# Optimization experiments

Measured on AMD Instinct MI355X. Metric: run time of the kernel, lower is better.

The kernel has to match this reference:

```python
import jax, jax.numpy as jnp
import numpy as np

B, S, D, H = 2, 2048, 768, 12
DK = D // H
NEG = -1000000000.0


def setup_inputs() -> dict:
    key = jax.random.key(0)
    ks = jax.random.split(key, 12)
    inp = {
        "query": jax.random.normal(ks[0], (B, S, D), jnp.float32),
        "key": jax.random.normal(ks[1], (B, S, D), jnp.float32),
        "value": jax.random.normal(ks[2], (B, S, D), jnp.float32),
        "mask": jax.random.randint(ks[3], (B, 1, 1, S), 0, 2, jnp.int32),
    }
    sc = 1.0 / np.sqrt(D)
    inp["Wq"] = jax.random.normal(ks[4], (D, D), jnp.float32) * sc
    inp["bq"] = jnp.zeros((D,), jnp.float32)
    inp["Wk"] = jax.random.normal(ks[5], (D, D), jnp.float32) * sc
    inp["bk"] = jnp.zeros((D,), jnp.float32)
    inp["Wv"] = jax.random.normal(ks[6], (D, D), jnp.float32) * sc
    inp["bv"] = jnp.zeros((D,), jnp.float32)
    inp["Wo"] = jax.random.normal(ks[7], (D, D), jnp.float32) * sc
    inp["bo"] = jnp.zeros((D,), jnp.float32)
    return inp


def reference(query, key, value, mask, Wq, bq, Wk, bk, Wv, bv, Wo, bo):
    b = query.shape[0]
    # QKV projections -> [B, H, S, DK]
    def proj(x, W, bias):
        y = jnp.einsum('bsd,de->bse', x, W.T) + bias
        return y.reshape(b, -1, H, DK).transpose(0, 2, 1, 3)
    q = proj(query, Wq, bq)
    k = proj(key, Wk, bk)
    v = proj(value, Wv, bv)
    # scores: [B, H, S, S]
    scores = jnp.einsum('bhqd,bhkd->bhqk', q, k) / jnp.sqrt(jnp.float32(DK))
    scores = jnp.where(mask == 0, jnp.float32(NEG), scores)
    p = jax.nn.softmax(scores, axis=-1)
    x = jnp.einsum('bhqk,bhkd->bhqd', p, v)  # [B, H, S, DK]
    x = x.transpose(0, 2, 1, 3).reshape(b, -1, H * DK)
    return jnp.einsum('bsd,de->bse', x, Wo.T) + bo
```

## Files before the change

kernel.cpp:

```cpp
#include <hip/hip_runtime.h>

typedef unsigned short u16;
typedef __attribute__((ext_vector_type(8))) __bf16 bf16x8;
typedef __attribute__((ext_vector_type(8))) short s16x8;
typedef __attribute__((ext_vector_type(8))) unsigned short u16x8;
typedef __attribute__((ext_vector_type(4))) float f32x4;
typedef __attribute__((ext_vector_type(4))) unsigned short u16x4;
typedef __attribute__((ext_vector_type(4))) float fl4;

#define MFMA(a, b, c) __builtin_amdgcn_mfma_f32_16x16x32_bf16((a), (b), (c), 0, 0, 0)
#define QSC 0.18033688011112042f

__device__ __forceinline__ u16 f2bf(float f) {
  union { float f; unsigned u; } v; v.f = f;
  unsigned u = v.u;
  return (u16)((u + 0x7fffu + ((u >> 16) & 1u)) >> 16);
}

__device__ __forceinline__ float bf2f(u16 u) {
  union { unsigned u; float f; } v; v.u = ((unsigned)u) << 16;
  return v.f;
}

__device__ __forceinline__ void gll16(const u16* g, u16* l) {
  typedef __attribute__((address_space(1))) unsigned int gu32;
  typedef __attribute__((address_space(3))) unsigned int lu32;
  __builtin_amdgcn_global_load_lds((gu32*)g, (lu32*)l, 16, 0, 0);
}


__global__ __launch_bounds__(256) void k_convert_x(
    const float* __restrict__ q, const float* __restrict__ k,
    const float* __restrict__ v, u16* __restrict__ xb) {
  const int NG = 4096 * 768 / 4;
  const int n = 3 * NG;
  for (int i = blockIdx.x * 256 + threadIdx.x; i < n; i += gridDim.x * 256) {
    int seg = i / NG;
    int j = (i - seg * NG) * 4;
    const float* s = (seg == 0) ? q : ((seg == 1) ? k : v);
    fl4 f = *(const fl4*)(s + j);
    u16x4 o;
    o[0] = f2bf(f[0]); o[1] = f2bf(f[1]); o[2] = f2bf(f[2]); o[3] = f2bf(f[3]);
    *(u16x4*)(xb + seg * (4096 * 768) + j) = o;
  }
}

__global__ __launch_bounds__(256) void k_convert_w(
    const float* __restrict__ Wq, const float* __restrict__ Wk,
    const float* __restrict__ Wv, const float* __restrict__ Wo,
    u16* __restrict__ wqkv, u16* __restrict__ wob) {
  const int n = 3072 * 192;
  for (int i = blockIdx.x * 256 + threadIdx.x; i < n; i += gridDim.x * 256) {
    int row = i / 192;
    int col = (i - row * 192) * 4;
    const float* src; u16* dst; float sc = 1.0f;
    if (row < 768)       { src = Wq + row * 768;          dst = wqkv + row * 768; sc = QSC; }
    else if (row < 1536) { src = Wk + (row - 768) * 768;  dst = wqkv + row * 768; }
    else if (row < 2304) { src = Wv + (row - 1536) * 768; dst = wqkv + row * 768; }
    else                 { src = Wo + (row - 2304) * 768; dst = wob + (row - 2304) * 768; }
    fl4 f = *(const fl4*)(src + col);
    u16x4 o;
    o[0] = f2bf(f[0] * sc); o[1] = f2bf(f[1] * sc);
    o[2] = f2bf(f[2] * sc); o[3] = f2bf(f[3] * sc);
    *(u16x4*)(dst + col) = o;
  }
}


__global__ __launch_bounds__(256) void k_gemm_qkv(
    const u16* __restrict__ xb, const u16* __restrict__ wqkv,
    const float* __restrict__ bq, const float* __restrict__ bk_,
    const float* __restrict__ bv_,
    u16* __restrict__ Qb, u16* __restrict__ Kb, u16* __restrict__ Vtb) {
  __shared__ __align__(16) u16 As[128 * 32];
  __shared__ __align__(16) u16 Bs[128 * 32];
  const int tid = threadIdx.x;
  const int row0 = blockIdx.x * 128, col0 = blockIdx.y * 128;
  const int seg = col0 / 768;
  const u16* A = xb + (size_t)seg * (4096 * 768);
  const int w = tid >> 6, lane = tid & 63, lr = lane & 15, kg = lane >> 4;
  const int wr = (w >> 1) * 64, wc = (w & 1) * 64;

  const int c0 = tid, c1 = tid + 256;
  const int r0c = c0 >> 2, p0 = c0 & 3, g0 = p0 ^ ((r0c >> 1) & 3);
  const int r1c = c1 >> 2, p1 = c1 & 3, g1 = p1 ^ ((r1c >> 1) & 3);

  f32x4 acc[4][4];
  f32x4 zero = {0.f, 0.f, 0.f, 0.f};
#pragma unroll
  for (int i = 0; i < 4; i++)
#pragma unroll
    for (int j = 0; j < 4; j++) acc[i][j] = zero;

  int aoff[4], boff[4];
#pragma unroll
  for (int mi = 0; mi < 4; mi++) {
    int r = wr + mi * 16 + lr;
    aoff[mi] = r * 32 + (kg ^ ((r >> 1) & 3)) * 8;
  }
#pragma unroll
  for (int ni = 0; ni < 4; ni++) {
    int r = wc + ni * 16 + lr;
    boff[ni] = r * 32 + (kg ^ ((r >> 1) & 3)) * 8;
  }

  for (int kt = 0; kt < 24; kt++) {
    const int k0 = kt * 32;
    gll16(A + (row0 + r0c) * 768 + k0 + g0 * 8, As + c0 * 8);
    gll16(A + (row0 + r1c) * 768 + k0 + g1 * 8, As + c1 * 8);
    gll16(wqkv + (col0 + r0c) * 768 + k0 + g0 * 8, Bs + c0 * 8);
    gll16(wqkv + (col0 + r1c) * 768 + k0 + g1 * 8, Bs + c1 * 8);
    __syncthreads();
    bf16x8 af[4], bfr[4];
#pragma unroll
    for (int mi = 0; mi < 4; mi++) af[mi] = *(const bf16x8*)(As + aoff[mi]);
#pragma unroll
    for (int ni = 0; ni < 4; ni++) bfr[ni] = *(const bf16x8*)(Bs + boff[ni]);
#pragma unroll
    for (int mi = 0; mi < 4; mi++)
#pragma unroll
      for (int ni = 0; ni < 4; ni++)
        acc[mi][ni] = MFMA(af[mi], bfr[ni], acc[mi][ni]);
    __syncthreads();
  }

  const float* bias = (seg == 0) ? bq : ((seg == 1) ? bk_ : bv_);
  const float bsc = (seg == 0) ? QSC : 1.0f;
  const int ncol0 = col0 - seg * 768;
#pragma unroll
  for (int ni = 0; ni < 4; ni++) {
    const int n = ncol0 + wc + ni * 16 + lr;
    const float bval = bias[n] * bsc;
    const int hh = n >> 6, dk = n & 63;
#pragma unroll
    for (int mi = 0; mi < 4; mi++)
#pragma unroll
      for (int j = 0; j < 4; j++) {
        const int m = row0 + wr + mi * 16 + kg * 4 + j;
        const int bb = m >> 11, ss = m & 2047;
        const u16 val = f2bf(acc[mi][ni][j] + bval);
        if (seg == 0)
          Qb[((size_t)((bb * 12 + hh) * 2048 + ss)) * 64 + dk] = val;
        else if (seg == 1)
          Kb[((size_t)((bb * 12 + hh) * 2048 + ss)) * 64 + dk] = val;
        else
          Vtb[((size_t)((bb * 12 + hh) * 64 + dk)) * 2048 + ss] = val;
      }
  }
}


__global__ __launch_bounds__(256) void k_attn(
    const u16* __restrict__ Qb, const u16* __restrict__ Kb,
    const u16* __restrict__ Vtb, const int* __restrict__ mask,
    u16* __restrict__ o_part, float* __restrict__ l_part) {
  __shared__ __align__(16) u16 Ks[64 * 64];
  __shared__ __align__(16) u16 Vs[64 * 64];
  __shared__ __align__(16) u16 Ps[4][32 * 64];
  const int bh = blockIdx.y, b = bh / 12;
  const int half = blockIdx.z;
  const int kvb = half << 10;
  const int tid = threadIdx.x, w = tid >> 6, lane = tid & 63;
  const int lr = lane & 15, g = lane >> 4;
  const int q0 = blockIdx.x * 128 + w * 32;
  const u16* Qh = Qb + (size_t)bh * (2048 * 64);
  const u16* Kh = Kb + (size_t)bh * (2048 * 64);
  const u16* Vh = Vtb + (size_t)bh * (64 * 2048);
  const int* mb = mask + b * 2048;
  u16* Pw = Ps[w];

  bf16x8 aq[2][2];
#pragma unroll
  for (int mi = 0; mi < 2; mi++)
#pragma unroll
    for (int ks = 0; ks < 2; ks++)
      aq[mi][ks] = *(const bf16x8*)(Qh + (q0 + mi * 16 + lr) * 64 + ks * 32 + g * 8);

  f32x4 zero = {0.f, 0.f, 0.f, 0.f};
  f32x4 o[2][4];
#pragma unroll
  for (int mi = 0; mi < 2; mi++)
#pragma unroll
    for (int di = 0; di < 4; di++) o[mi][di] = zero;
  f32x4 o_l[2];
  o_l[0] = zero; o_l[1] = zero;

  s16x8 ov = {0x3F80, 0x3F80, 0x3F80, 0x3F80, 0x3F80, 0x3F80, 0x3F80, 0x3F80};
  bf16x8 ones = __builtin_bit_cast(bf16x8, ov);

  const int c0 = tid, c1 = tid + 256;
  const int sr0 = c0 >> 3, sg0 = (c0 & 7) ^ (sr0 & 7);
  const int sr1 = c1 >> 3, sg1 = (c1 & 7) ^ (sr1 & 7);

  for (int t = 0; t < 16; t++) {
    const int kv0 = kvb + t * 64;
    gll16(Kh + (kv0 + sr0) * 64 + sg0 * 8, Ks + c0 * 8);
    gll16(Kh + (kv0 + sr1) * 64 + sg1 * 8, Ks + c1 * 8);
    gll16(Vh + sr0 * 2048 + kv0 + sg0 * 8, Vs + c0 * 8);
    gll16(Vh + sr1 * 2048 + kv0 + sg1 * 8, Vs + c1 * 8);
    __syncthreads();

    f32x4 s[2][4];
#pragma unroll
    for (int ni = 0; ni < 4; ni++) {
      const int row = ni * 16 + lr;
      bf16x8 b0 = *(const bf16x8*)(Ks + row * 64 + ((g ^ (row & 7)) << 3));
      bf16x8 b1 = *(const bf16x8*)(Ks + row * 64 + (((4 + g) ^ (row & 7)) << 3));
#pragma unroll
      for (int mi = 0; mi < 2; mi++) {
        f32x4 z = zero;
        z = MFMA(aq[mi][0], b0, z);
        z = MFMA(aq[mi][1], b1, z);
        s[mi][ni] = z;
      }
    }
    int mk[4];
#pragma unroll
    for (int ni = 0; ni < 4; ni++) mk[ni] = mb[kv0 + ni * 16 + lr];
#pragma unroll
    for (int mi = 0; mi < 2; mi++)
#pragma unroll
      for (int ni = 0; ni < 4; ni++)
#pragma unroll
        for (int j = 0; j < 4; j++)
          s[mi][ni][j] = mk[ni] ? s[mi][ni][j] : -1e9f;

#pragma unroll
    for (int mi = 0; mi < 2; mi++)
#pragma unroll
      for (int ni = 0; ni < 4; ni++)
#pragma unroll
        for (int j = 0; j < 4; j++) {
          const float p = __builtin_amdgcn_exp2f(s[mi][ni][j]);
          const int prow = mi * 16 + g * 4 + j;
          const int byt = prow * 128 + ((ni * 32 + lr * 2) ^ ((prow & 7) << 4));
          Pw[byt >> 1] = f2bf(p);
        }

#pragma unroll
    for (int ks2 = 0; ks2 < 2; ks2++) {
      bf16x8 ap[2];
#pragma unroll
      for (int mi = 0; mi < 2; mi++) {
        const int prow = mi * 16 + lr;
        const int byt = prow * 128 + ((ks2 * 64 + g * 16) ^ ((prow & 7) << 4));
        ap[mi] = *(const bf16x8*)(Pw + (byt >> 1));
      }
#pragma unroll
      for (int di = 0; di < 4; di++) {
        const int vrow = di * 16 + lr;
        bf16x8 bv = *(const bf16x8*)(Vs + vrow * 64 + (((ks2 * 4 + g) ^ (vrow & 7)) << 3));
#pragma unroll
        for (int mi = 0; mi < 2; mi++)
          o[mi][di] = MFMA(ap[mi], bv, o[mi][di]);
      }
#pragma unroll
      for (int mi = 0; mi < 2; mi++)
        o_l[mi] = MFMA(ap[mi], ones, o_l[mi]);
    }
    __syncthreads();
  }

  u16* opw = o_part + (size_t)(half * 24 + bh) * (2048 * 64);
  float* lpw = l_part + (size_t)(half * 24 + bh) * 2048;
#pragma unroll
  for (int mi = 0; mi < 2; mi++) {
#pragma unroll
    for (int di = 0; di < 4; di++)
#pragma unroll
      for (int j = 0; j < 4; j++) {
        const int row = q0 + mi * 16 + g * 4 + j;
        opw[(size_t)row * 64 + di * 16 + lr] = f2bf(o[mi][di][j]);
      }
    if (lr == 0) {
#pragma unroll
      for (int j = 0; j < 4; j++)
        lpw[q0 + mi * 16 + g * 4 + j] = o_l[mi][j];
    }
  }
}


__global__ __launch_bounds__(256) void k_combine(
    const u16* __restrict__ o_part, const float* __restrict__ l_part,
    u16* __restrict__ attn) {
  const int idx = blockIdx.x * 256 + threadIdx.x;
  const int row = idx >> 3;
  const int c8 = (idx & 7) << 3;
  const size_t HALF_O = (size_t)24 * 2048 * 64;
  u16x8 a0 = *(const u16x8*)(o_part + (size_t)row * 64 + c8);
  u16x8 a1 = *(const u16x8*)(o_part + HALF_O + (size_t)row * 64 + c8);
  const float l = l_part[row] + l_part[24 * 2048 + row];
  const float rcp = 1.0f / l;
  u16x8 r;
#pragma unroll
  for (int j = 0; j < 8; j++)
    r[j] = f2bf((bf2f(a0[j]) + bf2f(a1[j])) * rcp);
  const int bh = row >> 11, s = row & 2047;
  const int b = bh / 12, h = bh - b * 12;
  *(u16x8*)(attn + (size_t)(b * 2048 + s) * 768 + h * 64 + c8) = r;
}


__global__ __launch_bounds__(256) void k_gemm_out(
    const u16* __restrict__ attn, const u16* __restrict__ wob,
    const float* __restrict__ bo, float* __restrict__ out) {
  __shared__ __align__(16) u16 As[128 * 32];
  __shared__ __align__(16) u16 Bs[128 * 32];
  const int tid = threadIdx.x;
  const int row0 = blockIdx.x * 128, col0 = blockIdx.y * 128;
  const int w = tid >> 6, lane = tid & 63, lr = lane & 15, kg = lane >> 4;
  const int wr = (w >> 1) * 64, wc = (w & 1) * 64;

  const int c0 = tid, c1 = tid + 256;
  const int r0c = c0 >> 2, p0 = c0 & 3, g0 = p0 ^ ((r0c >> 1) & 3);
  const int r1c = c1 >> 2, p1 = c1 & 3, g1 = p1 ^ ((r1c >> 1) & 3);

  f32x4 acc[4][4];
  f32x4 zero = {0.f, 0.f, 0.f, 0.f};
#pragma unroll
  for (int i = 0; i < 4; i++)
#pragma unroll
    for (int j = 0; j < 4; j++) acc[i][j] = zero;

  int aoff[4], boff[4];
#pragma unroll
  for (int mi = 0; mi < 4; mi++) {
    int r = wr + mi * 16 + lr;
    aoff[mi] = r * 32 + (kg ^ ((r >> 1) & 3)) * 8;
  }
#pragma unroll
  for (int ni = 0; ni < 4; ni++) {
    int r = wc + ni * 16 + lr;
    boff[ni] = r * 32 + (kg ^ ((r >> 1) & 3)) * 8;
  }

  for (int kt = 0; kt < 24; kt++) {
    const int k0 = kt * 32;
    gll16(attn + (row0 + r0c) * 768 + k0 + g0 * 8, As + c0 * 8);
    gll16(attn + (row0 + r1c) * 768 + k0 + g1 * 8, As + c1 * 8);
    gll16(wob + (col0 + r0c) * 768 + k0 + g0 * 8, Bs + c0 * 8);
    gll16(wob + (col0 + r1c) * 768 + k0 + g1 * 8, Bs + c1 * 8);
    __syncthreads();
    bf16x8 af[4], bfr[4];
#pragma unroll
    for (int mi = 0; mi < 4; mi++) af[mi] = *(const bf16x8*)(As + aoff[mi]);
#pragma unroll
    for (int ni = 0; ni < 4; ni++) bfr[ni] = *(const bf16x8*)(Bs + boff[ni]);
#pragma unroll
    for (int mi = 0; mi < 4; mi++)
#pragma unroll
      for (int ni = 0; ni < 4; ni++)
        acc[mi][ni] = MFMA(af[mi], bfr[ni], acc[mi][ni]);
    __syncthreads();
  }

#pragma unroll
  for (int ni = 0; ni < 4; ni++) {
    const int n = col0 + wc + ni * 16 + lr;
    const float bval = bo[n];
#pragma unroll
    for (int mi = 0; mi < 4; mi++)
#pragma unroll
      for (int j = 0; j < 4; j++) {
        const int m = row0 + wr + mi * 16 + kg * 4 + j;
        out[(size_t)m * 768 + n] = acc[mi][ni][j] + bval;
      }
  }
}


extern "C" void kernel_launch(void* const* d_in, const int* in_sizes, int n_in,
                              void* d_out, int out_size, void* d_ws, size_t ws_size,
                              hipStream_t stream) {
  const float* q = (const float*)d_in[0];
  const float* k = (const float*)d_in[1];
  const float* v = (const float*)d_in[2];
  const int* mask = (const int*)d_in[3];
  const float* Wq = (const float*)d_in[4];
  const float* bq = (const float*)d_in[5];
  const float* Wk = (const float*)d_in[6];
  const float* bk = (const float*)d_in[7];
  const float* Wv = (const float*)d_in[8];
  const float* bv = (const float*)d_in[9];
  const float* Wo = (const float*)d_in[10];
  const float* bo = (const float*)d_in[11];
  float* out = (float*)d_out;

  u16* xb = (u16*)d_ws;
  u16* wqkv = xb + (size_t)3 * 4096 * 768;
  u16* wob = wqkv + (size_t)2304 * 768;
  u16* Qb = wob + (size_t)768 * 768;
  u16* Kb = Qb + (size_t)4096 * 768;
  u16* Vtb = Kb + (size_t)4096 * 768;
  u16* attn = Vtb + (size_t)4096 * 768;

  u16* o_part = xb;
  float* l_part = (float*)(xb + (size_t)2 * 24 * 2048 * 64);

  k_convert_x<<<dim3(4608), dim3(256), 0, stream>>>(q, k, v, xb);
  k_convert_w<<<dim3(2304), dim3(256), 0, stream>>>(Wq, Wk, Wv, Wo, wqkv, wob);
  k_gemm_qkv<<<dim3(32, 18), dim3(256), 0, stream>>>(xb, wqkv, bq, bk, bv, Qb, Kb, Vtb);
  k_attn<<<dim3(16, 24, 2), dim3(256), 0, stream>>>(Qb, Kb, Vtb, mask, o_part, l_part);
  k_combine<<<dim3(1536), dim3(256), 0, stream>>>(o_part, l_part, attn);
  k_gemm_out<<<dim3(32, 6), dim3(256), 0, stream>>>(attn, wob, bo, out);
}
```

Before: 130.7 us.

## Double-buffer K/V tiles in LDS and stage mask in shared memory

The attention kernel now uses two LDS buffers for K and V. It prefetches the next 64-key tile with async global-to-LDS loads while the current tile is being computed, which removes one of the two barriers per iteration. The mask slice for the block's key half is loaded into LDS once at kernel start, so the kernel no longer issues per-iteration global mask loads. The cost is more LDS per block (about 52KB), which can lower occupancy, and correctness now depends on the end-of-iteration barrier waiting for the outstanding LDS-direct loads.

```diff
diff --git a/kernel.cpp b/kernel.cpp
--- a/kernel.cpp
+++ b/kernel.cpp
@@ -7,6 +7,7 @@
 typedef __attribute__((ext_vector_type(4))) float f32x4;
 typedef __attribute__((ext_vector_type(4))) unsigned short u16x4;
 typedef __attribute__((ext_vector_type(4))) float fl4;
+typedef __attribute__((ext_vector_type(4))) int i32x4;
 
 #define MFMA(a, b, c) __builtin_amdgcn_mfma_f32_16x16x32_bf16((a), (b), (c), 0, 0, 0)
 #define QSC 0.18033688011112042f
@@ -154,9 +155,10 @@
     const u16* __restrict__ Qb, const u16* __restrict__ Kb,
     const u16* __restrict__ Vtb, const int* __restrict__ mask,
     u16* __restrict__ o_part, float* __restrict__ l_part) {
-  __shared__ __align__(16) u16 Ks[64 * 64];
-  __shared__ __align__(16) u16 Vs[64 * 64];
+  __shared__ __align__(16) u16 Ks[2][64 * 64];
+  __shared__ __align__(16) u16 Vs[2][64 * 64];
   __shared__ __align__(16) u16 Ps[4][32 * 64];
+  __shared__ __align__(16) int mlds[1024];
   const int bh = blockIdx.y, b = bh / 12;
   const int half = blockIdx.z;
   const int kvb = half << 10;
@@ -169,6 +171,8 @@
   const int* mb = mask + b * 2048;
   u16* Pw = Ps[w];
 
+  *(i32x4*)(mlds + tid * 4) = *(const i32x4*)(mb + kvb + tid * 4);
+
   bf16x8 aq[2][2];
 #pragma unroll
   for (int mi = 0; mi < 2; mi++)
@@ -191,21 +195,31 @@
   const int c0 = tid, c1 = tid + 256;
   const int sr0 = c0 >> 3, sg0 = (c0 & 7) ^ (sr0 & 7);
   const int sr1 = c1 >> 3, sg1 = (c1 & 7) ^ (sr1 & 7);
+  const u16* kA0 = Kh + (size_t)kvb * 64 + sr0 * 64 + sg0 * 8;
+  const u16* kA1 = Kh + (size_t)kvb * 64 + sr1 * 64 + sg1 * 8;
+  const u16* vA0 = Vh + sr0 * 2048 + kvb + sg0 * 8;
+  const u16* vA1 = Vh + sr1 * 2048 + kvb + sg1 * 8;
+
+#define STAGE(u) { u16* kd = Ks[(u)&1]; u16* vd = Vs[(u)&1];           \
+    gll16(kA0 + (u) * 4096, kd + c0 * 8);                              \
+    gll16(kA1 + (u) * 4096, kd + c1 * 8);                              \
+    gll16(vA0 + (u) * 64,  vd + c0 * 8);                               \
+    gll16(vA1 + (u) * 64,  vd + c1 * 8); }
+
+  STAGE(0);
+  __syncthreads();
 
   for (int t = 0; t < 16; t++) {
-    const int kv0 = kvb + t * 64;
-    gll16(Kh + (kv0 + sr0) * 64 + sg0 * 8, Ks + c0 * 8);
-    gll16(Kh + (kv0 + sr1) * 64 + sg1 * 8, Ks + c1 * 8);
-    gll16(Vh + sr0 * 2048 + kv0 + sg0 * 8, Vs + c0 * 8);
-    gll16(Vh + sr1 * 2048 + kv0 + sg1 * 8, Vs + c1 * 8);
-    __syncthreads();
+    if (t < 15) STAGE(t + 1);
+    const u16* Kc = Ks[t & 1];
+    const u16* Vc = Vs[t & 1];
 
     f32x4 s[2][4];
 #pragma unroll
     for (int ni = 0; ni < 4; ni++) {
       const int row = ni * 16 + lr;
-      bf16x8 b0 = *(const bf16x8*)(Ks + row * 64 + ((g ^ (row & 7)) << 3));
-      bf16x8 b1 = *(const bf16x8*)(Ks + row * 64 + (((4 + g) ^ (row & 7)) << 3));
+      bf16x8 b0 = *(const bf16x8*)(Kc + row * 64 + ((g ^ (row & 7)) << 3));
+      bf16x8 b1 = *(const bf16x8*)(Kc + row * 64 + (((4 + g) ^ (row & 7)) << 3));
 #pragma unroll
       for (int mi = 0; mi < 2; mi++) {
         f32x4 z = zero;
@@ -216,7 +230,7 @@
     }
     int mk[4];
 #pragma unroll
-    for (int ni = 0; ni < 4; ni++) mk[ni] = mb[kv0 + ni * 16 + lr];
+    for (int ni = 0; ni < 4; ni++) mk[ni] = mlds[t * 64 + ni * 16 + lr];
 #pragma unroll
     for (int mi = 0; mi < 2; mi++)
 #pragma unroll
@@ -249,7 +263,7 @@
 #pragma unroll
       for (int di = 0; di < 4; di++) {
         const int vrow = di * 16 + lr;
-        bf16x8 bv = *(const bf16x8*)(Vs + vrow * 64 + (((ks2 * 4 + g) ^ (vrow & 7)) << 3));
+        bf16x8 bv = *(const bf16x8*)(Vc + vrow * 64 + (((ks2 * 4 + g) ^ (vrow & 7)) << 3));
 #pragma unroll
         for (int mi = 0; mi < 2; mi++)
           o[mi][di] = MFMA(ap[mi], bv, o[mi][di]);
@@ -258,8 +272,10 @@
       for (int mi = 0; mi < 2; mi++)
         o_l[mi] = MFMA(ap[mi], ones, o_l[mi]);
     }
-    __syncthreads();
-  }
+
+    if (t < 15) __syncthreads();
+  }
+#undef STAGE
 
   u16* opw = o_part + (size_t)(half * 24 + bh) * (2048 * 64);
   float* lpw = l_part + (size_t)(half * 24 + bh) * 2048;
```

After: 123.7 us. -5.3%, faster.
